# Optimization experiments

Measured on AMD Instinct MI355X. Metric: run time of the kernel, lower is better.

## Reference

```python
import jax, jax.numpy as jnp
import numpy as np

N_NODES = 50000
N_EDGES = 800000
D = 64  # in_feat == hidden_channels


def _param(key, shape, fan_in):
    return jax.random.normal(key, shape, dtype=jnp.float32) / np.sqrt(fan_in)


def setup_inputs() -> dict:
    key = jax.random.key(0)
    ks = jax.random.split(key, 32)
    inp = {
        "x": jax.random.normal(ks[0], (N_NODES, D), dtype=jnp.float32),
        "edge_index": jax.random.randint(ks[1], (2, N_EDGES), 0, N_NODES, dtype=jnp.int64),
    }
    i = 2
    for l in (1, 2, 3):
        inp[f"W1_{l}"] = _param(ks[i + 0], (D, D), D)   # LEConv lin1 (source nodes)
        inp[f"b1_{l}"] = jnp.zeros((D,), jnp.float32)
        inp[f"W2_{l}"] = _param(ks[i + 1], (D, D), D)   # LEConv lin2 (target nodes, no bias)
        inp[f"W3_{l}"] = _param(ks[i + 2], (D, D), D)   # LEConv lin3 (root/self)
        inp[f"b3_{l}"] = jnp.zeros((D,), jnp.float32)
        inp[f"Wl_{l}"] = _param(ks[i + 3], (D, D), D)   # post-conv Linear
        inp[f"bl_{l}"] = jnp.zeros((D,), jnp.float32)
        i += 4
    return inp


def _leconv(x, src, dst, W1, b1, W2, W3, b3):
    # out_i = lin3(x_i) + sum_{j->i} (lin1(x_j) - lin2(x_i))
    a = x @ W1 + b1          # [N, D]
    b = x @ W2               # [N, D]
    msg = a[src] - b[dst]    # [E, D]  gather + elementwise
    agg = jax.ops.segment_sum(msg, dst, num_segments=x.shape[0])  # scatter-add
    return agg + (x @ W3 + b3)


def reference(x, edge_index,
              W1_1, b1_1, W2_1, W3_1, b3_1, Wl_1, bl_1,
              W1_2, b1_2, W2_2, W3_2, b3_2, Wl_2, bl_2,
              W1_3, b1_3, W2_3, W3_3, b3_3, Wl_3, bl_3):
    src, dst = edge_index[0], edge_index[1]
    h = x
    for (W1, b1, W2, W3, b3, Wl, bl) in (
        (W1_1, b1_1, W2_1, W3_1, b3_1, Wl_1, bl_1),
        (W1_2, b1_2, W2_2, W3_2, b3_2, Wl_2, bl_2),
        (W1_3, b1_3, W2_3, W3_3, b3_3, Wl_3, bl_3),
    ):
        h = _leconv(h, src, dst, W1, b1, W2, W3, b3)
        h = jax.nn.relu(h @ Wl + bl)
    return h
```

## Files before the change

### kernel.cpp

```cpp
#include <hip/hip_runtime.h>

#define N_NODES 50000
#define N_EDGES 800000
#define SCAN_NB ((N_NODES + 255) / 256)
#define NCHUNK 128
#define NRANGE 4
#define RNODES (N_NODES / NRANGE)
#define CEDGES (N_EDGES / NCHUNK)
#define HIST_NB (NCHUNK * NRANGE)

typedef __attribute__((ext_vector_type(8))) short short8;
typedef __attribute__((ext_vector_type(4))) float f32x4;

struct LPtrs { const float *W1, *W2, *W3, *Wl, *b1, *b3, *bl; };
struct AllPtrs { LPtrs l[3]; };

__device__ inline unsigned short f2b(float f) {
    union { float f; unsigned u; } c; c.f = f;
    return (unsigned short)((c.u + 0x7FFFu + ((c.u >> 16) & 1u)) >> 16);
}
__device__ inline float b2f(unsigned short h) {
    union { unsigned u; float f; } c; c.u = ((unsigned)h) << 16;
    return c.f;
}

__global__ __launch_bounds__(256) void histpack_kernel(const int* __restrict__ dst,
                                                       unsigned char* __restrict__ hist_part,
                                                       AllPtrs ap,
                                                       unsigned short* __restrict__ Wp,
                                                       float* __restrict__ rows) {
    __shared__ int h[RNODES];
    const int t = threadIdx.x;
    if (blockIdx.x < HIST_NB) {
        const int chunk = blockIdx.x >> 2;
        const int range = blockIdx.x & 3;
        const int nbase = range * RNODES;
        for (int i = t; i < RNODES; i += 256) h[i] = 0;
        __syncthreads();
        const int* dp = dst + chunk * CEDGES;
        for (int i = t; i < CEDGES; i += 256) {
            int d = dp[i] - nbase;
            if ((unsigned)d < (unsigned)RNODES) atomicAdd(&h[d], 1);
        }
        __syncthreads();
        unsigned char* out = hist_part + (long)chunk * N_NODES + nbase;
        for (int i = t; i < RNODES; i += 256) out[i] = (unsigned char)h[i];
    } else {
        float* sW = (float*)h;
        float* sL = (float*)h + 64 * 65;
        const int wi = blockIdx.x - HIST_NB;
        const int layer = wi / 12;
        const int ct = wi % 12;
        LPtrs L = ap.l[layer];
        const float* Wm = (ct < 4) ? L.W1 : (ct < 8) ? L.W2 : L.W3;
        const int colb = (ct & 3) * 16;
        for (int i = t; i < 64 * 64; i += 256) sW[(i >> 6) * 65 + (i & 63)] = Wm[i];
        for (int i = t; i < 64 * 16; i += 256) {
            int q = i >> 4, c = i & 15;
            sL[q * 17 + c] = L.Wl[q * 64 + colb + c];
        }
        __syncthreads();
        for (int local = t; local < 1024; local += 256) {
            int j = local & 7, lane = (local >> 3) & 63, s = local >> 9;
            int k = s * 32 + (lane >> 4) * 8 + j;
            int c = lane & 15;
            float acc = 0.f;
            #pragma unroll 8
            for (int q = 0; q < 64; ++q) acc += sW[k * 65 + q] * sL[q * 17 + c];
            Wp[layer * 12288 + ct * 1024 + local] = f2b(acc);
        }
        if (ct == 0 && t < 64) {
            int col = t;
            float r1 = 0.f, r3 = 0.f;
            for (int q = 0; q < 64; ++q) {
                float wl = L.Wl[q * 64 + col];
                r1 += L.b1[q] * wl;
                r3 += L.b3[q] * wl;
            }
            rows[layer * 128 + col] = r1;
            rows[layer * 128 + 64 + col] = r3 + L.bl[col];
        }
    }
}

__global__ __launch_bounds__(256) void scanA2_kernel(unsigned char* __restrict__ hist_part,
                                                     int* __restrict__ off,
                                                     int* __restrict__ deg,
                                                     int* __restrict__ bsum) {
    __shared__ int tmp[256];
    const int t = threadIdx.x;
    const int node = blockIdx.x * 256 + t;
    int run = 0;
    if (node < N_NODES) {
        #pragma unroll
        for (int c = 0; c < NCHUNK; ++c) {
            unsigned char* p = hist_part + (long)c * N_NODES + node;
            int v = *p;
            *p = (unsigned char)run;
            run += v;
        }
        deg[node] = run;
    }
    int v = run;
    tmp[t] = v;
    __syncthreads();
    #pragma unroll
    for (int d = 1; d < 256; d <<= 1) {
        int u = (t >= d) ? tmp[t - d] : 0;
        __syncthreads();
        tmp[t] += u;
        __syncthreads();
    }
    if (node < N_NODES) off[node] = tmp[t] - v;
    if (t == 255) bsum[blockIdx.x] = tmp[255];
}

__global__ __launch_bounds__(256) void fillp_kernel(const int* __restrict__ src,
                                                    const int* __restrict__ dst,
                                                    const int* __restrict__ off,
                                                    const int* __restrict__ bsum,
                                                    int* __restrict__ boff,
                                                    const unsigned char* __restrict__ hist_part,
                                                    int* __restrict__ csr) {
    __shared__ int cur[RNODES];
    __shared__ int sb[256];
    const int t = threadIdx.x;
    int v = (t < SCAN_NB) ? bsum[t] : 0;
    sb[t] = v;
    __syncthreads();
    #pragma unroll
    for (int d = 1; d < 256; d <<= 1) {
        int u = (t >= d) ? sb[t - d] : 0;
        __syncthreads();
        sb[t] += u;
        __syncthreads();
    }
    int excl = sb[t] - v;
    __syncthreads();
    sb[t] = excl;
    if (blockIdx.x == 0 && t < SCAN_NB) boff[t] = excl;
    __syncthreads();

    const int chunk = blockIdx.x >> 2;
    const int range = blockIdx.x & 3;
    const int nbase = range * RNODES;
    const unsigned char* bp = hist_part + (long)chunk * N_NODES + nbase;
    const int* op = off + nbase;
    for (int i = t; i < RNODES; i += 256)
        cur[i] = op[i] + sb[(nbase + i) >> 8] + (int)bp[i];
    __syncthreads();
    const int* dp = dst + chunk * CEDGES;
    const int* sp = src + chunk * CEDGES;
    for (int i = t; i < CEDGES; i += 256) {
        int d = dp[i] - nbase;
        if ((unsigned)d < (unsigned)RNODES) {
            int pos = atomicAdd(&cur[d], 1);
            csr[pos] = sp[i];
        }
    }
}

__global__ __launch_bounds__(256) void gemm3w_kernel(
    const unsigned short* __restrict__ hbf, const float* __restrict__ hf32,
    const unsigned short* __restrict__ Wp,
    const int* __restrict__ deg, const float* __restrict__ rows,
    unsigned short* __restrict__ abf, unsigned short* __restrict__ wbf, int n)
{
    const int t = threadIdx.x;
    const int lane = t & 63;
    const int quad = lane >> 4, lm = lane & 15;
    const int row_base = blockIdx.x * 64 + (t >> 6) * 16;

    int arow = min(row_base + lm, n - 1);
    short8 a0, a1;
    if (hf32) {
        const float* hrow = hf32 + (long)arow * 64;
        #pragma unroll
        for (int j = 0; j < 8; ++j) {
            a0[j] = (short)f2b(hrow[quad * 8 + j]);
            a1[j] = (short)f2b(hrow[32 + quad * 8 + j]);
        }
    } else {
        const unsigned short* hrow = hbf + (long)arow * 64;
        a0 = *(const short8*)(hrow + quad * 8);
        a1 = *(const short8*)(hrow + 32 + quad * 8);
    }

    const short8* wp = (const short8*)Wp;
    f32x4 acc[12];
    #pragma unroll
    for (int ct = 0; ct < 12; ++ct) {
        f32x4 z = {0.f, 0.f, 0.f, 0.f};
        short8 w0 = wp[(ct * 2 + 0) * 64 + lane];
        short8 w1 = wp[(ct * 2 + 1) * 64 + lane];
        z = __builtin_amdgcn_mfma_f32_16x16x32_bf16(a0, w0, z, 0, 0, 0);
        z = __builtin_amdgcn_mfma_f32_16x16x32_bf16(a1, w1, z, 0, 0, 0);
        acc[ct] = z;
    }

    const int g0 = row_base + quad * 4;
    float dg[4];
    #pragma unroll
    for (int r = 0; r < 4; ++r) dg[r] = (float)deg[min(g0 + r, n - 1)];

    #pragma unroll
    for (int ct = 0; ct < 4; ++ct) {
        int col = ct * 16 + lm;
        float r1 = rows[col];
        float r3 = rows[64 + col];
        #pragma unroll
        for (int r = 0; r < 4; ++r) {
            int g = g0 + r;
            if (g < n) {
                abf[(long)g * 64 + col] = f2b(acc[ct][r]);
                float wv = acc[8 + ct][r] - dg[r] * (acc[4 + ct][r] - r1) + r3;
                wbf[(long)g * 64 + col] = f2b(wv);
            }
        }
    }
}

__global__ __launch_bounds__(256) void gather_out_kernel(
    const int* __restrict__ off, const int* __restrict__ boff,
    const int* __restrict__ degv, const int* __restrict__ csr,
    const unsigned short* __restrict__ abf,
    const unsigned short* __restrict__ wbf,
    float* __restrict__ out_f, unsigned short* __restrict__ out_b, int last)
{
    int node = blockIdx.x * 4 + (threadIdx.x >> 6);
    int lane = threadIdx.x & 63;
    const int g = lane >> 4;
    const int f = (lane & 15) * 4;
    int beg = off[node] + boff[node >> 8];
    int end = beg + degv[node];
    float ax = 0.f, ay = 0.f, az = 0.f, aw = 0.f;
    int j = beg;
    for (; j + 16 <= end; j += 16) {
        int s0 = csr[j + g], s1 = csr[j + 4 + g];
        int s2 = csr[j + 8 + g], s3 = csr[j + 12 + g];
        ushort4 v0 = *(const ushort4*)(abf + (long)s0 * 64 + f);
        ushort4 v1 = *(const ushort4*)(abf + (long)s1 * 64 + f);
        ushort4 v2 = *(const ushort4*)(abf + (long)s2 * 64 + f);
        ushort4 v3 = *(const ushort4*)(abf + (long)s3 * 64 + f);
        ax += b2f(v0.x) + b2f(v1.x) + b2f(v2.x) + b2f(v3.x);
        ay += b2f(v0.y) + b2f(v1.y) + b2f(v2.y) + b2f(v3.y);
        az += b2f(v0.z) + b2f(v1.z) + b2f(v2.z) + b2f(v3.z);
        aw += b2f(v0.w) + b2f(v1.w) + b2f(v2.w) + b2f(v3.w);
    }
    for (; j + 8 <= end; j += 8) {
        int s0 = csr[j + g], s1 = csr[j + 4 + g];
        ushort4 v0 = *(const ushort4*)(abf + (long)s0 * 64 + f);
        ushort4 v1 = *(const ushort4*)(abf + (long)s1 * 64 + f);
        ax += b2f(v0.x) + b2f(v1.x);
        ay += b2f(v0.y) + b2f(v1.y);
        az += b2f(v0.z) + b2f(v1.z);
        aw += b2f(v0.w) + b2f(v1.w);
    }
    for (; j < end; j += 4) {
        int jj = j + g;
        if (jj < end) {
            int s0 = csr[jj];
            ushort4 v0 = *(const ushort4*)(abf + (long)s0 * 64 + f);
            ax += b2f(v0.x); ay += b2f(v0.y); az += b2f(v0.z); aw += b2f(v0.w);
        }
    }
    #pragma unroll
    for (int m = 16; m < 64; m <<= 1) {
        ax += __shfl_xor(ax, m, 64);
        ay += __shfl_xor(ay, m, 64);
        az += __shfl_xor(az, m, 64);
        aw += __shfl_xor(aw, m, 64);
    }
    if (g == 0) {
        ushort4 wv = *(const ushort4*)(wbf + (long)node * 64 + f);
        float o0 = fmaxf(ax + b2f(wv.x), 0.f);
        float o1 = fmaxf(ay + b2f(wv.y), 0.f);
        float o2 = fmaxf(az + b2f(wv.z), 0.f);
        float o3 = fmaxf(aw + b2f(wv.w), 0.f);
        if (last) {
            float4 o = {o0, o1, o2, o3};
            *(float4*)(out_f + (long)node * 64 + f) = o;
        } else {
            ushort4 o;
            o.x = f2b(o0); o.y = f2b(o1); o.z = f2b(o2); o.w = f2b(o3);
            *(ushort4*)(out_b + (long)node * 64 + f) = o;
        }
    }
}

extern "C" void kernel_launch(void* const* d_in, const int* in_sizes, int n_in,
                              void* d_out, int out_size, void* d_ws, size_t ws_size,
                              hipStream_t stream) {
    const float* x  = (const float*)d_in[0];
    const int*   ei = (const int*)d_in[1];
    const int*   src = ei;
    const int*   dst = ei + N_EDGES;

    char* wsb = (char*)d_ws;
    unsigned char*  hist_part = (unsigned char*)(wsb);
    unsigned short* abf  = (unsigned short*)(wsb + 12800000);
    unsigned short* wbf  = (unsigned short*)(wsb + 19200000);
    unsigned short* h1   = (unsigned short*)(wsb + 25600000);
    unsigned short* Wp   = (unsigned short*)(wsb + 38400000);
    float*          rows = (float*)(wsb + 38500000);
    int* off  = (int*)(wsb + 38600000);
    int* deg  = off + N_NODES;
    int* bsum = deg + N_NODES;
    int* boff = bsum + SCAN_NB;
    int* csr  = boff + SCAN_NB;

    const int NBLK = (N_NODES + 63) / 64;

    AllPtrs ap;
    for (int l = 0; l < 3; ++l) {
        int base = 2 + l * 7;
        ap.l[l].W1 = (const float*)d_in[base + 0];
        ap.l[l].b1 = (const float*)d_in[base + 1];
        ap.l[l].W2 = (const float*)d_in[base + 2];
        ap.l[l].W3 = (const float*)d_in[base + 3];
        ap.l[l].b3 = (const float*)d_in[base + 4];
        ap.l[l].Wl = (const float*)d_in[base + 5];
        ap.l[l].bl = (const float*)d_in[base + 6];
    }

    histpack_kernel<<<HIST_NB + 36, 256, 0, stream>>>(dst, hist_part, ap, Wp, rows);
    scanA2_kernel<<<SCAN_NB, 256, 0, stream>>>(hist_part, off, deg, bsum);
    fillp_kernel<<<HIST_NB, 256, 0, stream>>>(src, dst, off, bsum, boff,
                                              hist_part, csr);

    const unsigned short* hin = nullptr;
    for (int l = 0; l < 3; ++l) {
        const unsigned short* wp = Wp + l * 12288;
        gemm3w_kernel<<<NBLK, 256, 0, stream>>>(
            hin, (l == 0) ? x : nullptr, wp, deg, rows + l * 128,
            abf, wbf, N_NODES);

        int last = (l == 2);
        gather_out_kernel<<<N_NODES / 4, 256, 0, stream>>>(
            off, boff, deg, csr, abf, wbf, (float*)d_out, h1, last);
        hin = h1;
    }
}
```

Measured before the change: 258.3 us.

## Fuse CSR fill with layer-1 GEMM and restructure histogram and scan

The layer-1 GEMM blocks now run inside the same launch as the CSR fill, which removes one kernel launch and lets the two independent pieces of work overlap. The histogram now packs four 8-bit counters per 32-bit shared atomic and writes words instead of bytes. The number of edge chunks is halved, so the per-node column scan reads fewer entries, and that scan is split across four thread groups per 64-node block. In exchange, each fill block loops over more block sums serially, and 8-bit counter packing relies on per-chunk degrees staying below 256.

```diff
diff --git a/kernel.cpp b/kernel.cpp
--- a/kernel.cpp
+++ b/kernel.cpp
@@ -2,12 +2,12 @@
 
 #define N_NODES 50000
 #define N_EDGES 800000
-#define SCAN_NB ((N_NODES + 255) / 256)
-#define NCHUNK 128
+#define NCHUNK 64
 #define NRANGE 4
 #define RNODES (N_NODES / NRANGE)
 #define CEDGES (N_EDGES / NCHUNK)
 #define HIST_NB (NCHUNK * NRANGE)
+#define SCAN_NB2 ((N_NODES + 63) / 64)
 
 typedef __attribute__((ext_vector_type(8))) short short8;
 typedef __attribute__((ext_vector_type(4))) float f32x4;
@@ -29,22 +29,23 @@
                                                        AllPtrs ap,
                                                        unsigned short* __restrict__ Wp,
                                                        float* __restrict__ rows) {
-    __shared__ int h[RNODES];
+    __shared__ unsigned int h[5248];
     const int t = threadIdx.x;
     if (blockIdx.x < HIST_NB) {
         const int chunk = blockIdx.x >> 2;
         const int range = blockIdx.x & 3;
         const int nbase = range * RNODES;
-        for (int i = t; i < RNODES; i += 256) h[i] = 0;
+        for (int i = t; i < RNODES / 4; i += 256) h[i] = 0u;
         __syncthreads();
         const int* dp = dst + chunk * CEDGES;
         for (int i = t; i < CEDGES; i += 256) {
             int d = dp[i] - nbase;
-            if ((unsigned)d < (unsigned)RNODES) atomicAdd(&h[d], 1);
-        }
-        __syncthreads();
-        unsigned char* out = hist_part + (long)chunk * N_NODES + nbase;
-        for (int i = t; i < RNODES; i += 256) out[i] = (unsigned char)h[i];
+            if ((unsigned)d < (unsigned)RNODES)
+                atomicAdd(&h[d >> 2], 1u << ((d & 3) * 8));
+        }
+        __syncthreads();
+        unsigned int* out = (unsigned int*)(hist_part + (long)chunk * N_NODES + nbase);
+        for (int i = t; i < RNODES / 4; i += 256) out[i] = h[i];
     } else {
         float* sW = (float*)h;
         float* sL = (float*)h + 64 * 65;
@@ -87,59 +88,155 @@
                                                      int* __restrict__ off,
                                                      int* __restrict__ deg,
                                                      int* __restrict__ bsum) {
-    __shared__ int tmp[256];
+    __shared__ int part[4][64];
     const int t = threadIdx.x;
-    const int node = blockIdx.x * 256 + t;
-    int run = 0;
+    const int ln = t & 63;
+    const int cg = t >> 6;
+    const int node = blockIdx.x * 64 + ln;
+    unsigned char* col = hist_part + node;
+    unsigned char v[16];
+    int s = 0;
     if (node < N_NODES) {
         #pragma unroll
-        for (int c = 0; c < NCHUNK; ++c) {
-            unsigned char* p = hist_part + (long)c * N_NODES + node;
-            int v = *p;
-            *p = (unsigned char)run;
-            run += v;
-        }
-        deg[node] = run;
-    }
-    int v = run;
-    tmp[t] = v;
+        for (int k = 0; k < 16; ++k) {
+            v[k] = col[(long)(cg * 16 + k) * N_NODES];
+            s += v[k];
+        }
+    }
+    part[cg][ln] = s;
     __syncthreads();
-    #pragma unroll
-    for (int d = 1; d < 256; d <<= 1) {
-        int u = (t >= d) ? tmp[t - d] : 0;
-        __syncthreads();
-        tmp[t] += u;
-        __syncthreads();
-    }
-    if (node < N_NODES) off[node] = tmp[t] - v;
-    if (t == 255) bsum[blockIdx.x] = tmp[255];
-}
-
-__global__ __launch_bounds__(256) void fillp_kernel(const int* __restrict__ src,
-                                                    const int* __restrict__ dst,
-                                                    const int* __restrict__ off,
-                                                    const int* __restrict__ bsum,
-                                                    int* __restrict__ boff,
-                                                    const unsigned char* __restrict__ hist_part,
-                                                    int* __restrict__ csr) {
+    int run = 0, tot = 0;
+    #pragma unroll
+    for (int g = 0; g < 4; ++g) {
+        int p = part[g][ln];
+        if (g < cg) run += p;
+        tot += p;
+    }
+    if (node < N_NODES) {
+        #pragma unroll
+        for (int k = 0; k < 16; ++k) {
+            col[(long)(cg * 16 + k) * N_NODES] = (unsigned char)run;
+            run += v[k];
+        }
+        if (cg == 0) deg[node] = tot;
+    }
+    if (cg == 0) {
+        int x = tot;
+        #pragma unroll
+        for (int d = 1; d < 64; d <<= 1) {
+            int u = __shfl_up(x, d, 64);
+            if (ln >= d) x += u;
+        }
+        if (node < N_NODES) off[node] = x - tot;
+        if (ln == 63) bsum[blockIdx.x] = x;
+    }
+}
+
+__device__ __forceinline__ void gemm_body(int blk, int t,
+    const unsigned short* __restrict__ hbf, const float* __restrict__ hf32,
+    const unsigned short* __restrict__ Wp,
+    const int* __restrict__ deg, const float* __restrict__ rows,
+    unsigned short* __restrict__ abf, unsigned short* __restrict__ wbf, int n)
+{
+    const int lane = t & 63;
+    const int quad = lane >> 4, lm = lane & 15;
+    const int row_base = blk * 64 + (t >> 6) * 16;
+
+    int arow = min(row_base + lm, n - 1);
+    short8 a0, a1;
+    if (hf32) {
+        const float* hrow = hf32 + (long)arow * 64;
+        #pragma unroll
+        for (int j = 0; j < 8; ++j) {
+            a0[j] = (short)f2b(hrow[quad * 8 + j]);
+            a1[j] = (short)f2b(hrow[32 + quad * 8 + j]);
+        }
+    } else {
+        const unsigned short* hrow = hbf + (long)arow * 64;
+        a0 = *(const short8*)(hrow + quad * 8);
+        a1 = *(const short8*)(hrow + 32 + quad * 8);
+    }
+
+    const short8* wp = (const short8*)Wp;
+    f32x4 acc[12];
+    #pragma unroll
+    for (int ct = 0; ct < 12; ++ct) {
+        f32x4 z = {0.f, 0.f, 0.f, 0.f};
+        short8 w0 = wp[(ct * 2 + 0) * 64 + lane];
+        short8 w1 = wp[(ct * 2 + 1) * 64 + lane];
+        z = __builtin_amdgcn_mfma_f32_16x16x32_bf16(a0, w0, z, 0, 0, 0);
+        z = __builtin_amdgcn_mfma_f32_16x16x32_bf16(a1, w1, z, 0, 0, 0);
+        acc[ct] = z;
+    }
+
+    const int g0 = row_base + quad * 4;
+    float dg[4];
+    #pragma unroll
+    for (int r = 0; r < 4; ++r) dg[r] = (float)deg[min(g0 + r, n - 1)];
+
+    #pragma unroll
+    for (int ct = 0; ct < 4; ++ct) {
+        int col = ct * 16 + lm;
+        float r1 = rows[col];
+        float r3 = rows[64 + col];
+        #pragma unroll
+        for (int r = 0; r < 4; ++r) {
+            int g = g0 + r;
+            if (g < n) {
+                abf[(long)g * 64 + col] = f2b(acc[ct][r]);
+                float wv = acc[8 + ct][r] - dg[r] * (acc[4 + ct][r] - r1) + r3;
+                wbf[(long)g * 64 + col] = f2b(wv);
+            }
+        }
+    }
+}
+
+__global__ __launch_bounds__(256) void gemm3w_kernel(
+    const unsigned short* __restrict__ hbf, const float* __restrict__ hf32,
+    const unsigned short* __restrict__ Wp,
+    const int* __restrict__ deg, const float* __restrict__ rows,
+    unsigned short* __restrict__ abf, unsigned short* __restrict__ wbf, int n)
+{
+    gemm_body(blockIdx.x, threadIdx.x, hbf, hf32, Wp, deg, rows, abf, wbf, n);
+}
+
+__global__ __launch_bounds__(256) void fillgemm_kernel(
+    const int* __restrict__ src, const int* __restrict__ dst,
+    const int* __restrict__ off, const int* __restrict__ bsum,
+    int* __restrict__ boff, const unsigned char* __restrict__ hist_part,
+    int* __restrict__ csr,
+    const float* __restrict__ x, const unsigned short* __restrict__ Wp,
+    const int* __restrict__ deg, const float* __restrict__ rows,
+    unsigned short* __restrict__ abf, unsigned short* __restrict__ wbf)
+{
     __shared__ int cur[RNODES];
-    __shared__ int sb[256];
+    __shared__ int sb[SCAN_NB2 + 2];
+    if (blockIdx.x >= HIST_NB) {
+        gemm_body(blockIdx.x - HIST_NB, threadIdx.x, nullptr, x, Wp, deg, rows,
+                  abf, wbf, N_NODES);
+        return;
+    }
     const int t = threadIdx.x;
-    int v = (t < SCAN_NB) ? bsum[t] : 0;
-    sb[t] = v;
-    __syncthreads();
-    #pragma unroll
-    for (int d = 1; d < 256; d <<= 1) {
-        int u = (t >= d) ? sb[t - d] : 0;
-        __syncthreads();
-        sb[t] += u;
-        __syncthreads();
-    }
-    int excl = sb[t] - v;
-    __syncthreads();
-    sb[t] = excl;
-    if (blockIdx.x == 0 && t < SCAN_NB) boff[t] = excl;
-    __syncthreads();
+
+    int carry = 0;
+    for (int base = 0; base < SCAN_NB2; base += 256) {
+        int idx = base + t;
+        int v = (idx < SCAN_NB2) ? bsum[idx] : 0;
+        cur[t] = v;
+        __syncthreads();
+        #pragma unroll
+        for (int d = 1; d < 256; d <<= 1) {
+            int u = (t >= d) ? cur[t - d] : 0;
+            __syncthreads();
+            cur[t] += u;
+            __syncthreads();
+        }
+        if (idx < SCAN_NB2) sb[idx] = carry + cur[t] - v;
+        carry += cur[255];
+        __syncthreads();
+    }
+    if (blockIdx.x == 0)
+        for (int i = t; i < SCAN_NB2; i += 256) boff[i] = sb[i];
 
     const int chunk = blockIdx.x >> 2;
     const int range = blockIdx.x & 3;
@@ -147,7 +244,7 @@
     const unsigned char* bp = hist_part + (long)chunk * N_NODES + nbase;
     const int* op = off + nbase;
     for (int i = t; i < RNODES; i += 256)
-        cur[i] = op[i] + sb[(nbase + i) >> 8] + (int)bp[i];
+        cur[i] = op[i] + sb[(nbase + i) >> 6] + (int)bp[i];
     __syncthreads();
     const int* dp = dst + chunk * CEDGES;
     const int* sp = src + chunk * CEDGES;
@@ -156,66 +253,6 @@
         if ((unsigned)d < (unsigned)RNODES) {
             int pos = atomicAdd(&cur[d], 1);
             csr[pos] = sp[i];
-        }
-    }
-}
-
-__global__ __launch_bounds__(256) void gemm3w_kernel(
-    const unsigned short* __restrict__ hbf, const float* __restrict__ hf32,
-    const unsigned short* __restrict__ Wp,
-    const int* __restrict__ deg, const float* __restrict__ rows,
-    unsigned short* __restrict__ abf, unsigned short* __restrict__ wbf, int n)
-{
-    const int t = threadIdx.x;
-    const int lane = t & 63;
-    const int quad = lane >> 4, lm = lane & 15;
-    const int row_base = blockIdx.x * 64 + (t >> 6) * 16;
-
-    int arow = min(row_base + lm, n - 1);
-    short8 a0, a1;
-    if (hf32) {
-        const float* hrow = hf32 + (long)arow * 64;
-        #pragma unroll
-        for (int j = 0; j < 8; ++j) {
-            a0[j] = (short)f2b(hrow[quad * 8 + j]);
-            a1[j] = (short)f2b(hrow[32 + quad * 8 + j]);
-        }
-    } else {
-        const unsigned short* hrow = hbf + (long)arow * 64;
-        a0 = *(const short8*)(hrow + quad * 8);
-        a1 = *(const short8*)(hrow + 32 + quad * 8);
-    }
-
-    const short8* wp = (const short8*)Wp;
-    f32x4 acc[12];
-    #pragma unroll
-    for (int ct = 0; ct < 12; ++ct) {
-        f32x4 z = {0.f, 0.f, 0.f, 0.f};
-        short8 w0 = wp[(ct * 2 + 0) * 64 + lane];
-        short8 w1 = wp[(ct * 2 + 1) * 64 + lane];
-        z = __builtin_amdgcn_mfma_f32_16x16x32_bf16(a0, w0, z, 0, 0, 0);
-        z = __builtin_amdgcn_mfma_f32_16x16x32_bf16(a1, w1, z, 0, 0, 0);
-        acc[ct] = z;
-    }
-
-    const int g0 = row_base + quad * 4;
-    float dg[4];
-    #pragma unroll
-    for (int r = 0; r < 4; ++r) dg[r] = (float)deg[min(g0 + r, n - 1)];
-
-    #pragma unroll
-    for (int ct = 0; ct < 4; ++ct) {
-        int col = ct * 16 + lm;
-        float r1 = rows[col];
-        float r3 = rows[64 + col];
-        #pragma unroll
-        for (int r = 0; r < 4; ++r) {
-            int g = g0 + r;
-            if (g < n) {
-                abf[(long)g * 64 + col] = f2b(acc[ct][r]);
-                float wv = acc[8 + ct][r] - dg[r] * (acc[4 + ct][r] - r1) + r3;
-                wbf[(long)g * 64 + col] = f2b(wv);
-            }
         }
     }
 }
@@ -231,7 +268,7 @@
     int lane = threadIdx.x & 63;
     const int g = lane >> 4;
     const int f = (lane & 15) * 4;
-    int beg = off[node] + boff[node >> 8];
+    int beg = off[node] + boff[node >> 6];
     int end = beg + degv[node];
     float ax = 0.f, ay = 0.f, az = 0.f, aw = 0.f;
     int j = beg;
@@ -306,8 +343,8 @@
     int* off  = (int*)(wsb + 38600000);
     int* deg  = off + N_NODES;
     int* bsum = deg + N_NODES;
-    int* boff = bsum + SCAN_NB;
-    int* csr  = boff + SCAN_NB;
+    int* boff = bsum + 1024;
+    int* csr  = boff + 1024;
 
     const int NBLK = (N_NODES + 63) / 64;
 
@@ -324,20 +361,21 @@
     }
 
     histpack_kernel<<<HIST_NB + 36, 256, 0, stream>>>(dst, hist_part, ap, Wp, rows);
-    scanA2_kernel<<<SCAN_NB, 256, 0, stream>>>(hist_part, off, deg, bsum);
-    fillp_kernel<<<HIST_NB, 256, 0, stream>>>(src, dst, off, bsum, boff,
-                                              hist_part, csr);
-
-    const unsigned short* hin = nullptr;
-    for (int l = 0; l < 3; ++l) {
-        const unsigned short* wp = Wp + l * 12288;
+    scanA2_kernel<<<SCAN_NB2, 256, 0, stream>>>(hist_part, off, deg, bsum);
+    fillgemm_kernel<<<HIST_NB + NBLK, 256, 0, stream>>>(
+        src, dst, off, bsum, boff, hist_part, csr,
+        x, Wp, deg, rows, abf, wbf);
+
+    gather_out_kernel<<<N_NODES / 4, 256, 0, stream>>>(
+        off, boff, deg, csr, abf, wbf, (float*)d_out, h1, 0);
+
+    const unsigned short* hin = h1;
+    for (int l = 1; l < 3; ++l) {
         gemm3w_kernel<<<NBLK, 256, 0, stream>>>(
-            hin, (l == 0) ? x : nullptr, wp, deg, rows + l * 128,
+            hin, nullptr, Wp + l * 12288, deg, rows + l * 128,
             abf, wbf, N_NODES);
-
-        int last = (l == 2);
         gather_out_kernel<<<N_NODES / 4, 256, 0, stream>>>(
-            off, boff, deg, csr, abf, wbf, (float*)d_out, h1, last);
+            off, boff, deg, csr, abf, wbf, (float*)d_out, h1, (l == 2));
         hin = h1;
     }
 }
```

Measured after the change: 266.8 us. 1.03x slower.
